# Optimization experiments

Measured on AMD Instinct MI355X. Metric: run time of the kernel, lower is better.

Reference implementation:

```python
import jax, jax.numpy as jnp
import numpy as np

IN_FEATURES = 4096
PADDED_DIM = 4096
K_HALF = PADDED_DIM // 2 + 1  # 2049
K = K_HALF
ALPHA_INIT = 1.0
INIT_SCALE = 0.1
BIAS_SCALE = 0.1
BATCH = 8192


def setup_inputs() -> dict:
    key = jax.random.key(0)
    kx, kr, ki, kb = jax.random.split(key, 4)
    x = jax.random.normal(kx, (BATCH, IN_FEATURES), dtype=jnp.float32)
    # Params initialized as in the module's __init__ (frequency-decayed scale)
    k_idx = jnp.arange(K_HALF, dtype=jnp.float32)
    prior_s = 1.0 / jnp.sqrt(1.0 + k_idx ** ALPHA_INIT)
    w_real = jax.random.normal(kr, (K_HALF,), dtype=jnp.float32) * (INIT_SCALE * prior_s)
    w_imag = jax.random.normal(ki, (K_HALF,), dtype=jnp.float32) * (INIT_SCALE * prior_s)
    w_imag = w_imag.at[0].set(0.0)
    w_imag = w_imag.at[-1].set(0.0)  # Nyquist bin (padded_dim even)
    bias = jax.random.normal(kb, (PADDED_DIM,), dtype=jnp.float32) * BIAS_SCALE
    return {"x": x, "w_real": w_real, "w_imag": w_imag, "bias": bias}


def _fourier_full(w_real, w_imag):
    # Mask frequencies >= K, then build full-length spectrum via Hermitian symmetry.
    mask = (jnp.arange(K_HALF) < K).astype(w_real.dtype)
    half = w_real * mask + 1j * (w_imag * mask)  # [k_half] complex
    nyq = half[-1].real[None].astype(half.dtype)  # real Nyquist bin
    full = jnp.concatenate([half[:-1], nyq, jnp.conj(half[1:-1])[::-1]])  # [padded_dim]
    return full


def reference(x, w_real, w_imag, bias):
    fft_full = _fourier_full(w_real, w_imag)  # [padded_dim] complex64
    # d_in == padded_dim -> no zero-padding needed (slice is a no-op, kept faithful)
    x_pad = x[..., :PADDED_DIM]
    Xf = jnp.fft.fft(x_pad, axis=-1)                 # [B, padded_dim] complex
    y = jnp.fft.ifft(Xf * fft_full[None, :], axis=-1).real  # [B, padded_dim]
    return y + bias[None, :]
```

## Files before the change

kernel.cpp:

```cpp
#include <hip/hip_runtime.h>
#include <math.h>

#define N 4096
#define THREADS 256
#define BATCH 8192

#define SWZ(i) ((i) ^ (((i) >> 4) & 15))
#define IDX16(p) ((((p) & 3) << 2) | ((p) >> 2))

__device__ __forceinline__ float2 cmul(float2 a, float2 b) {
    return make_float2(fmaf(a.x, b.x, -(a.y * b.y)), fmaf(a.x, b.y, a.y * b.x));
}

template<bool INV>
__device__ __forceinline__ void dft4(float2* v, int base, int stride) {
    float2 a = v[base], b = v[base + stride], c = v[base + 2 * stride], d = v[base + 3 * stride];
    float2 t0 = make_float2(a.x + c.x, a.y + c.y);
    float2 t1 = make_float2(a.x - c.x, a.y - c.y);
    float2 t2 = make_float2(b.x + d.x, b.y + d.y);
    float2 t3 = make_float2(b.x - d.x, b.y - d.y);
    float2 j3 = INV ? make_float2(-t3.y, t3.x) : make_float2(t3.y, -t3.x);
    v[base]              = make_float2(t0.x + t2.x, t0.y + t2.y);
    v[base + stride]     = make_float2(t1.x + j3.x, t1.y + j3.y);
    v[base + 2 * stride] = make_float2(t0.x - t2.x, t0.y - t2.y);
    v[base + 3 * stride] = make_float2(t1.x - j3.x, t1.y - j3.y);
}

template<bool INV>
__device__ __forceinline__ void tw16(float2* v) {
    const float C1 = 0.9238795325112867f;
    const float S1 = 0.3826834323650898f;
    const float R2 = 0.7071067811865476f;
    const float s = INV ? 1.0f : -1.0f;
    const float2 W1 = make_float2(C1, s * S1);
    const float2 W2 = make_float2(R2, s * R2);
    const float2 W3 = make_float2(S1, s * C1);
    const float2 W6 = make_float2(-R2, s * R2);
    const float2 W9 = make_float2(-C1, -s * S1);
    v[5]  = cmul(v[5],  W1);
    v[9]  = cmul(v[9],  W2);
    v[13] = cmul(v[13], W3);
    v[6]  = cmul(v[6],  W2);
    { float2 z = v[10]; v[10] = INV ? make_float2(-z.y, z.x) : make_float2(z.y, -z.x); }
    v[14] = cmul(v[14], W6);
    v[7]  = cmul(v[7],  W3);
    v[11] = cmul(v[11], W6);
    v[15] = cmul(v[15], W9);
}

template<bool INV>
__device__ __forceinline__ void dft16(float2* v) {
    #pragma unroll
    for (int n1 = 0; n1 < 4; ++n1) dft4<INV>(v, n1, 4);
    tw16<INV>(v);
    #pragma unroll
    for (int k2 = 0; k2 < 4; ++k2) dft4<INV>(v, 4 * k2, 1);
}

template<bool INV>
__device__ __forceinline__ void dft16_perm(float2* v) {
    #pragma unroll
    for (int n1 = 0; n1 < 4; ++n1) dft4<INV>(v, 4 * n1, 1);
    tw16<INV>(v);
    #pragma unroll
    for (int k2 = 0; k2 < 4; ++k2) dft4<INV>(v, k2, 4);
}

__global__ void prep_kernel(const float* __restrict__ wr, const float* __restrict__ wi,
                            float2* __restrict__ H, float2* __restrict__ tw) {
    int i = blockIdx.x * blockDim.x + threadIdx.x;
    if (i < N) {
        double ang = -2.0 * M_PI * (double)i / (double)N;
        tw[i] = make_float2((float)cos(ang), (float)sin(ang));
        float re, im;
        if (i <= N / 2) {
            re = wr[i];
            im = (i == N / 2) ? 0.0f : wi[i];
        } else {
            re = wr[N - i];
            im = -wi[N - i];
        }
        H[i] = make_float2(re, im);
    }
}

__global__ void prep_twA_kernel(float2* __restrict__ twA) {
    int i = blockIdx.x * blockDim.x + threadIdx.x;
    int p = i >> 8, t = i & 255;
    double ang = -2.0 * M_PI * (double)(t * p) / (double)N;
    twA[i] = make_float2((float)cos(ang), (float)sin(ang));
}

__global__ __launch_bounds__(THREADS, 2) void fft_conv_kernel(
        const float* __restrict__ x, const float2* __restrict__ H,
        const float2* __restrict__ tw, const float2* __restrict__ twA,
        const float* __restrict__ bias, float* __restrict__ out) {
    __shared__ float2 lds[2 * N];
    float2* __restrict__ ldsA = lds;
    float2* __restrict__ ldsB = lds + N;
    const int t = threadIdx.x;
    const long base1 = (long)(4 * blockIdx.x) * N;
    const long base2 = base1 + N;
    const long base3 = base1 + 2 * N;
    const long base4 = base1 + 3 * N;

    float2 va[16], vb[16];

    #pragma unroll
    for (int r = 0; r < 16; ++r) {
        va[r].x = x[base1 + t + 256 * r];
        va[r].y = x[base2 + t + 256 * r];
    }
    #pragma unroll
    for (int r = 0; r < 16; ++r) {
        vb[r].x = x[base3 + t + 256 * r];
        vb[r].y = x[base4 + t + 256 * r];
    }

    dft16<false>(va);
    dft16<false>(vb);
    #pragma unroll
    for (int p = 1; p < 16; ++p) {
        float2 w = twA[p * 256 + t];
        va[IDX16(p)] = cmul(va[IDX16(p)], w);
        vb[IDX16(p)] = cmul(vb[IDX16(p)], w);
    }
    #pragma unroll
    for (int p = 0; p < 16; ++p) ldsA[SWZ(16 * t + p)] = va[IDX16(p)];
    #pragma unroll
    for (int p = 0; p < 16; ++p) ldsB[SWZ(16 * t + p)] = vb[IDX16(p)];
    __syncthreads();

    #pragma unroll
    for (int r = 0; r < 16; ++r) va[r] = ldsA[SWZ(t + 256 * r)];
    #pragma unroll
    for (int r = 0; r < 16; ++r) vb[r] = ldsB[SWZ(t + 256 * r)];
    __syncthreads();
    dft16<false>(va);
    dft16<false>(vb);
    {
        const int k = t & 15, j = t >> 4;
        #pragma unroll
        for (int p = 1; p < 16; ++p) {
            float2 w = tw[16 * j * p];
            va[IDX16(p)] = cmul(va[IDX16(p)], w);
            vb[IDX16(p)] = cmul(vb[IDX16(p)], w);
        }
        #pragma unroll
        for (int p = 0; p < 16; ++p) ldsA[SWZ(k + 256 * j + 16 * p)] = va[IDX16(p)];
        #pragma unroll
        for (int p = 0; p < 16; ++p) ldsB[SWZ(k + 256 * j + 16 * p)] = vb[IDX16(p)];
    }
    __syncthreads();

    #pragma unroll
    for (int r = 0; r < 16; ++r) va[r] = ldsA[SWZ(t + 256 * r)];
    #pragma unroll
    for (int r = 0; r < 16; ++r) vb[r] = ldsB[SWZ(t + 256 * r)];
    __syncthreads();
    dft16<false>(va);
    dft16<false>(vb);
    #pragma unroll
    for (int q = 0; q < 16; ++q) {
        float2 h = H[t + 256 * IDX16(q)];
        va[q] = cmul(va[q], h);
        vb[q] = cmul(vb[q], h);
    }

    dft16_perm<true>(va);
    dft16_perm<true>(vb);
    #pragma unroll
    for (int p = 1; p < 16; ++p) {
        float2 w = twA[p * 256 + t]; w.y = -w.y;
        va[p] = cmul(va[p], w);
        vb[p] = cmul(vb[p], w);
    }
    #pragma unroll
    for (int p = 0; p < 16; ++p) ldsA[SWZ(16 * t + p)] = va[p];
    #pragma unroll
    for (int p = 0; p < 16; ++p) ldsB[SWZ(16 * t + p)] = vb[p];
    __syncthreads();

    #pragma unroll
    for (int r = 0; r < 16; ++r) va[r] = ldsA[SWZ(t + 256 * r)];
    #pragma unroll
    for (int r = 0; r < 16; ++r) vb[r] = ldsB[SWZ(t + 256 * r)];
    __syncthreads();
    dft16<true>(va);
    dft16<true>(vb);
    {
        const int k = t & 15, j = t >> 4;
        #pragma unroll
        for (int p = 1; p < 16; ++p) {
            float2 w = tw[16 * j * p]; w.y = -w.y;
            va[IDX16(p)] = cmul(va[IDX16(p)], w);
            vb[IDX16(p)] = cmul(vb[IDX16(p)], w);
        }
        #pragma unroll
        for (int p = 0; p < 16; ++p) ldsA[SWZ(k + 256 * j + 16 * p)] = va[IDX16(p)];
        #pragma unroll
        for (int p = 0; p < 16; ++p) ldsB[SWZ(k + 256 * j + 16 * p)] = vb[IDX16(p)];
    }
    __syncthreads();

    #pragma unroll
    for (int r = 0; r < 16; ++r) va[r] = ldsA[SWZ(t + 256 * r)];
    #pragma unroll
    for (int r = 0; r < 16; ++r) vb[r] = ldsB[SWZ(t + 256 * r)];
    dft16<true>(va);
    dft16<true>(vb);
    const float inv = 1.0f / (float)N;
    #pragma unroll
    for (int p = 0; p < 16; ++p) {
        float2 a = va[IDX16(p)];
        float2 b = vb[IDX16(p)];
        float bb = bias[t + 256 * p];
        out[base1 + t + 256 * p] = fmaf(a.x, inv, bb);
        out[base2 + t + 256 * p] = fmaf(a.y, inv, bb);
        out[base3 + t + 256 * p] = fmaf(b.x, inv, bb);
        out[base4 + t + 256 * p] = fmaf(b.y, inv, bb);
    }
}

extern "C" void kernel_launch(void* const* d_in, const int* in_sizes, int n_in,
                              void* d_out, int out_size, void* d_ws, size_t ws_size,
                              hipStream_t stream) {
    const float* x  = (const float*)d_in[0];
    const float* wr = (const float*)d_in[1];
    const float* wi = (const float*)d_in[2];
    const float* bs = (const float*)d_in[3];
    float* out = (float*)d_out;

    float2* H   = (float2*)d_ws;
    float2* tw  = (float2*)((char*)d_ws + (size_t)N * sizeof(float2));
    float2* twA = (float2*)((char*)d_ws + (size_t)2 * N * sizeof(float2));

    prep_kernel<<<dim3(N / THREADS), dim3(THREADS), 0, stream>>>(wr, wi, H, tw);
    prep_twA_kernel<<<dim3(N / THREADS), dim3(THREADS), 0, stream>>>(twA);
    fft_conv_kernel<<<dim3(BATCH / 4), dim3(THREADS), 0, stream>>>(x, H, tw, twA, bs, out);
}
```

Baseline: 263.7 us.

## Stagger the two FFT streams so LDS exchanges overlap the other stream's compute

Reorders the kernel so the A and B FFT pipelines run offset by half a stage. While one buffer passes through an LDS transpose and barrier, the other stream's radix-16 butterflies run. Each buffer now has its own barrier, which removes the extra post-read syncs. Correctness depends on the two LDS buffers being independent, and the longer live ranges could raise register pressure under the 2-blocks launch bound.

```diff
diff --git a/kernel.cpp b/kernel.cpp
--- a/kernel.cpp
+++ b/kernel.cpp
@@ -99,6 +99,7 @@
     float2* __restrict__ ldsA = lds;
     float2* __restrict__ ldsB = lds + N;
     const int t = threadIdx.x;
+    const int k = t & 15, j = t >> 4;
     const long base1 = (long)(4 * blockIdx.x) * N;
     const long base2 = base1 + N;
     const long base3 = base1 + 2 * N;
@@ -118,105 +119,116 @@
     }
 
     dft16<false>(va);
+    #pragma unroll
+    for (int p = 1; p < 16; ++p)
+        va[IDX16(p)] = cmul(va[IDX16(p)], twA[p * 256 + t]);
+    #pragma unroll
+    for (int p = 0; p < 16; ++p) ldsA[SWZ(16 * t + p)] = va[IDX16(p)];
+    __syncthreads();
+
+    #pragma unroll
+    for (int r = 0; r < 16; ++r) va[r] = ldsA[SWZ(t + 256 * r)];
     dft16<false>(vb);
     #pragma unroll
-    for (int p = 1; p < 16; ++p) {
-        float2 w = twA[p * 256 + t];
-        va[IDX16(p)] = cmul(va[IDX16(p)], w);
-        vb[IDX16(p)] = cmul(vb[IDX16(p)], w);
-    }
-    #pragma unroll
-    for (int p = 0; p < 16; ++p) ldsA[SWZ(16 * t + p)] = va[IDX16(p)];
+    for (int p = 1; p < 16; ++p)
+        vb[IDX16(p)] = cmul(vb[IDX16(p)], twA[p * 256 + t]);
     #pragma unroll
     for (int p = 0; p < 16; ++p) ldsB[SWZ(16 * t + p)] = vb[IDX16(p)];
     __syncthreads();
 
     #pragma unroll
-    for (int r = 0; r < 16; ++r) va[r] = ldsA[SWZ(t + 256 * r)];
-    #pragma unroll
-    for (int r = 0; r < 16; ++r) vb[r] = ldsB[SWZ(t + 256 * r)];
-    __syncthreads();
+    for (int r = 0; r < 16; ++r) vb[r] = ldsB[SWZ(t + 256 * r)];
     dft16<false>(va);
+    #pragma unroll
+    for (int p = 1; p < 16; ++p)
+        va[IDX16(p)] = cmul(va[IDX16(p)], tw[16 * j * p]);
+    #pragma unroll
+    for (int p = 0; p < 16; ++p) ldsA[SWZ(k + 256 * j + 16 * p)] = va[IDX16(p)];
+    __syncthreads();
+
+    #pragma unroll
+    for (int r = 0; r < 16; ++r) va[r] = ldsA[SWZ(t + 256 * r)];
     dft16<false>(vb);
-    {
-        const int k = t & 15, j = t >> 4;
-        #pragma unroll
-        for (int p = 1; p < 16; ++p) {
-            float2 w = tw[16 * j * p];
-            va[IDX16(p)] = cmul(va[IDX16(p)], w);
-            vb[IDX16(p)] = cmul(vb[IDX16(p)], w);
-        }
-        #pragma unroll
-        for (int p = 0; p < 16; ++p) ldsA[SWZ(k + 256 * j + 16 * p)] = va[IDX16(p)];
-        #pragma unroll
-        for (int p = 0; p < 16; ++p) ldsB[SWZ(k + 256 * j + 16 * p)] = vb[IDX16(p)];
-    }
-    __syncthreads();
-
-    #pragma unroll
-    for (int r = 0; r < 16; ++r) va[r] = ldsA[SWZ(t + 256 * r)];
-    #pragma unroll
-    for (int r = 0; r < 16; ++r) vb[r] = ldsB[SWZ(t + 256 * r)];
-    __syncthreads();
+    #pragma unroll
+    for (int p = 1; p < 16; ++p)
+        vb[IDX16(p)] = cmul(vb[IDX16(p)], tw[16 * j * p]);
+    #pragma unroll
+    for (int p = 0; p < 16; ++p) ldsB[SWZ(k + 256 * j + 16 * p)] = vb[IDX16(p)];
+    __syncthreads();
+
+    #pragma unroll
+    for (int r = 0; r < 16; ++r) vb[r] = ldsB[SWZ(t + 256 * r)];
     dft16<false>(va);
-    dft16<false>(vb);
-    #pragma unroll
-    for (int q = 0; q < 16; ++q) {
-        float2 h = H[t + 256 * IDX16(q)];
-        va[q] = cmul(va[q], h);
-        vb[q] = cmul(vb[q], h);
-    }
-
+    #pragma unroll
+    for (int q = 0; q < 16; ++q)
+        va[q] = cmul(va[q], H[t + 256 * IDX16(q)]);
     dft16_perm<true>(va);
-    dft16_perm<true>(vb);
     #pragma unroll
     for (int p = 1; p < 16; ++p) {
         float2 w = twA[p * 256 + t]; w.y = -w.y;
         va[p] = cmul(va[p], w);
+    }
+    #pragma unroll
+    for (int p = 0; p < 16; ++p) ldsA[SWZ(16 * t + p)] = va[p];
+    __syncthreads();
+
+    #pragma unroll
+    for (int r = 0; r < 16; ++r) va[r] = ldsA[SWZ(t + 256 * r)];
+    dft16<false>(vb);
+    #pragma unroll
+    for (int q = 0; q < 16; ++q)
+        vb[q] = cmul(vb[q], H[t + 256 * IDX16(q)]);
+    dft16_perm<true>(vb);
+    #pragma unroll
+    for (int p = 1; p < 16; ++p) {
+        float2 w = twA[p * 256 + t]; w.y = -w.y;
         vb[p] = cmul(vb[p], w);
     }
     #pragma unroll
-    for (int p = 0; p < 16; ++p) ldsA[SWZ(16 * t + p)] = va[p];
-    #pragma unroll
     for (int p = 0; p < 16; ++p) ldsB[SWZ(16 * t + p)] = vb[p];
     __syncthreads();
 
     #pragma unroll
-    for (int r = 0; r < 16; ++r) va[r] = ldsA[SWZ(t + 256 * r)];
-    #pragma unroll
-    for (int r = 0; r < 16; ++r) vb[r] = ldsB[SWZ(t + 256 * r)];
-    __syncthreads();
+    for (int r = 0; r < 16; ++r) vb[r] = ldsB[SWZ(t + 256 * r)];
     dft16<true>(va);
+    #pragma unroll
+    for (int p = 1; p < 16; ++p) {
+        float2 w = tw[16 * j * p]; w.y = -w.y;
+        va[IDX16(p)] = cmul(va[IDX16(p)], w);
+    }
+    #pragma unroll
+    for (int p = 0; p < 16; ++p) ldsA[SWZ(k + 256 * j + 16 * p)] = va[IDX16(p)];
+    __syncthreads();
+
+    #pragma unroll
+    for (int r = 0; r < 16; ++r) va[r] = ldsA[SWZ(t + 256 * r)];
     dft16<true>(vb);
-    {
-        const int k = t & 15, j = t >> 4;
-        #pragma unroll
-        for (int p = 1; p < 16; ++p) {
-            float2 w = tw[16 * j * p]; w.y = -w.y;
-            va[IDX16(p)] = cmul(va[IDX16(p)], w);
-            vb[IDX16(p)] = cmul(vb[IDX16(p)], w);
-        }
-        #pragma unroll
-        for (int p = 0; p < 16; ++p) ldsA[SWZ(k + 256 * j + 16 * p)] = va[IDX16(p)];
-        #pragma unroll
-        for (int p = 0; p < 16; ++p) ldsB[SWZ(k + 256 * j + 16 * p)] = vb[IDX16(p)];
-    }
-    __syncthreads();
-
-    #pragma unroll
-    for (int r = 0; r < 16; ++r) va[r] = ldsA[SWZ(t + 256 * r)];
+    #pragma unroll
+    for (int p = 1; p < 16; ++p) {
+        float2 w = tw[16 * j * p]; w.y = -w.y;
+        vb[IDX16(p)] = cmul(vb[IDX16(p)], w);
+    }
+    #pragma unroll
+    for (int p = 0; p < 16; ++p) ldsB[SWZ(k + 256 * j + 16 * p)] = vb[IDX16(p)];
+    __syncthreads();
+
     #pragma unroll
     for (int r = 0; r < 16; ++r) vb[r] = ldsB[SWZ(t + 256 * r)];
     dft16<true>(va);
-    dft16<true>(vb);
     const float inv = 1.0f / (float)N;
     #pragma unroll
     for (int p = 0; p < 16; ++p) {
         float2 a = va[IDX16(p)];
-        float2 b = vb[IDX16(p)];
         float bb = bias[t + 256 * p];
         out[base1 + t + 256 * p] = fmaf(a.x, inv, bb);
         out[base2 + t + 256 * p] = fmaf(a.y, inv, bb);
+    }
+
+    dft16<true>(vb);
+    #pragma unroll
+    for (int p = 0; p < 16; ++p) {
+        float2 b = vb[IDX16(p)];
+        float bb = bias[t + 256 * p];
         out[base3 + t + 256 * p] = fmaf(b.x, inv, bb);
         out[base4 + t + 256 * p] = fmaf(b.y, inv, bb);
     }
```

Result: slower. 274.2 us (+4.0%).

## Make FFT-conv kernel persistent and prefetch next batch rows into registers

Applied to the files above, without the earlier changes.

The grid shrinks to 512 blocks, and each block loops over 4 groups of four rows. While the first LDS transpose of the current group is in flight, the block issues global loads for the next group into a separate register set (pa/pb). The goal is to hide global-memory latency behind compute. The cost is 64 extra float2 registers per thread, which may push register use past the occupancy target of 2 blocks per CU and cause spills. It also removes the wave-level parallelism that came from having more blocks.

```diff
diff --git a/kernel.cpp b/kernel.cpp
--- a/kernel.cpp
+++ b/kernel.cpp
@@ -4,6 +4,8 @@
 #define N 4096
 #define THREADS 256
 #define BATCH 8192
+#define GRID 512
+#define ITERS ((BATCH / 4) / GRID)
 
 #define SWZ(i) ((i) ^ (((i) >> 4) & 15))
 #define IDX16(p) ((((p) & 3) << 2) | ((p) >> 2))
@@ -99,47 +101,67 @@
     float2* __restrict__ ldsA = lds;
     float2* __restrict__ ldsB = lds + N;
     const int t = threadIdx.x;
-    const long base1 = (long)(4 * blockIdx.x) * N;
-    const long base2 = base1 + N;
-    const long base3 = base1 + 2 * N;
-    const long base4 = base1 + 3 * N;
-
+    const int k = t & 15, j = t >> 4;
+
+    float2 pa[16], pb[16];
     float2 va[16], vb[16];
 
-    #pragma unroll
-    for (int r = 0; r < 16; ++r) {
-        va[r].x = x[base1 + t + 256 * r];
-        va[r].y = x[base2 + t + 256 * r];
+    long g = blockIdx.x;
+
+    {
+        const long b1 = (long)(4 * g) * N, b2 = b1 + N, b3 = b1 + 2 * N, b4 = b1 + 3 * N;
+        #pragma unroll
+        for (int r = 0; r < 16; ++r) {
+            pa[r].x = x[b1 + t + 256 * r];
+            pa[r].y = x[b2 + t + 256 * r];
+        }
+        #pragma unroll
+        for (int r = 0; r < 16; ++r) {
+            pb[r].x = x[b3 + t + 256 * r];
+            pb[r].y = x[b4 + t + 256 * r];
+        }
     }
-    #pragma unroll
-    for (int r = 0; r < 16; ++r) {
-        vb[r].x = x[base3 + t + 256 * r];
-        vb[r].y = x[base4 + t + 256 * r];
-    }
-
-    dft16<false>(va);
-    dft16<false>(vb);
-    #pragma unroll
-    for (int p = 1; p < 16; ++p) {
-        float2 w = twA[p * 256 + t];
-        va[IDX16(p)] = cmul(va[IDX16(p)], w);
-        vb[IDX16(p)] = cmul(vb[IDX16(p)], w);
-    }
-    #pragma unroll
-    for (int p = 0; p < 16; ++p) ldsA[SWZ(16 * t + p)] = va[IDX16(p)];
-    #pragma unroll
-    for (int p = 0; p < 16; ++p) ldsB[SWZ(16 * t + p)] = vb[IDX16(p)];
-    __syncthreads();
-
-    #pragma unroll
-    for (int r = 0; r < 16; ++r) va[r] = ldsA[SWZ(t + 256 * r)];
-    #pragma unroll
-    for (int r = 0; r < 16; ++r) vb[r] = ldsB[SWZ(t + 256 * r)];
-    __syncthreads();
-    dft16<false>(va);
-    dft16<false>(vb);
-    {
-        const int k = t & 15, j = t >> 4;
+
+    #pragma unroll 1
+    for (int it = 0; it < ITERS; ++it) {
+        const long b1 = (long)(4 * g) * N, b2 = b1 + N, b3 = b1 + 2 * N, b4 = b1 + 3 * N;
+
+        dft16<false>(pa);
+        dft16<false>(pb);
+        #pragma unroll
+        for (int p = 1; p < 16; ++p) {
+            float2 w = twA[p * 256 + t];
+            pa[IDX16(p)] = cmul(pa[IDX16(p)], w);
+            pb[IDX16(p)] = cmul(pb[IDX16(p)], w);
+        }
+        #pragma unroll
+        for (int p = 0; p < 16; ++p) ldsA[SWZ(16 * t + p)] = pa[IDX16(p)];
+        #pragma unroll
+        for (int p = 0; p < 16; ++p) ldsB[SWZ(16 * t + p)] = pb[IDX16(p)];
+
+        if (it + 1 < ITERS) {
+            const long ng = g + GRID;
+            const long n1 = (long)(4 * ng) * N, n2 = n1 + N, n3 = n1 + 2 * N, n4 = n1 + 3 * N;
+            #pragma unroll
+            for (int r = 0; r < 16; ++r) {
+                pa[r].x = x[n1 + t + 256 * r];
+                pa[r].y = x[n2 + t + 256 * r];
+            }
+            #pragma unroll
+            for (int r = 0; r < 16; ++r) {
+                pb[r].x = x[n3 + t + 256 * r];
+                pb[r].y = x[n4 + t + 256 * r];
+            }
+        }
+        __syncthreads();
+
+        #pragma unroll
+        for (int r = 0; r < 16; ++r) va[r] = ldsA[SWZ(t + 256 * r)];
+        #pragma unroll
+        for (int r = 0; r < 16; ++r) vb[r] = ldsB[SWZ(t + 256 * r)];
+        __syncthreads();
+        dft16<false>(va);
+        dft16<false>(vb);
         #pragma unroll
         for (int p = 1; p < 16; ++p) {
             float2 w = tw[16 * j * p];
@@ -150,46 +172,42 @@
         for (int p = 0; p < 16; ++p) ldsA[SWZ(k + 256 * j + 16 * p)] = va[IDX16(p)];
         #pragma unroll
         for (int p = 0; p < 16; ++p) ldsB[SWZ(k + 256 * j + 16 * p)] = vb[IDX16(p)];
-    }
-    __syncthreads();
-
-    #pragma unroll
-    for (int r = 0; r < 16; ++r) va[r] = ldsA[SWZ(t + 256 * r)];
-    #pragma unroll
-    for (int r = 0; r < 16; ++r) vb[r] = ldsB[SWZ(t + 256 * r)];
-    __syncthreads();
-    dft16<false>(va);
-    dft16<false>(vb);
-    #pragma unroll
-    for (int q = 0; q < 16; ++q) {
-        float2 h = H[t + 256 * IDX16(q)];
-        va[q] = cmul(va[q], h);
-        vb[q] = cmul(vb[q], h);
-    }
-
-    dft16_perm<true>(va);
-    dft16_perm<true>(vb);
-    #pragma unroll
-    for (int p = 1; p < 16; ++p) {
-        float2 w = twA[p * 256 + t]; w.y = -w.y;
-        va[p] = cmul(va[p], w);
-        vb[p] = cmul(vb[p], w);
-    }
-    #pragma unroll
-    for (int p = 0; p < 16; ++p) ldsA[SWZ(16 * t + p)] = va[p];
-    #pragma unroll
-    for (int p = 0; p < 16; ++p) ldsB[SWZ(16 * t + p)] = vb[p];
-    __syncthreads();
-
-    #pragma unroll
-    for (int r = 0; r < 16; ++r) va[r] = ldsA[SWZ(t + 256 * r)];
-    #pragma unroll
-    for (int r = 0; r < 16; ++r) vb[r] = ldsB[SWZ(t + 256 * r)];
-    __syncthreads();
-    dft16<true>(va);
-    dft16<true>(vb);
-    {
-        const int k = t & 15, j = t >> 4;
+        __syncthreads();
+
+        #pragma unroll
+        for (int r = 0; r < 16; ++r) va[r] = ldsA[SWZ(t + 256 * r)];
+        #pragma unroll
+        for (int r = 0; r < 16; ++r) vb[r] = ldsB[SWZ(t + 256 * r)];
+        __syncthreads();
+        dft16<false>(va);
+        dft16<false>(vb);
+        #pragma unroll
+        for (int q = 0; q < 16; ++q) {
+            float2 h = H[t + 256 * IDX16(q)];
+            va[q] = cmul(va[q], h);
+            vb[q] = cmul(vb[q], h);
+        }
+        dft16_perm<true>(va);
+        dft16_perm<true>(vb);
+        #pragma unroll
+        for (int p = 1; p < 16; ++p) {
+            float2 w = twA[p * 256 + t]; w.y = -w.y;
+            va[p] = cmul(va[p], w);
+            vb[p] = cmul(vb[p], w);
+        }
+        #pragma unroll
+        for (int p = 0; p < 16; ++p) ldsA[SWZ(16 * t + p)] = va[p];
+        #pragma unroll
+        for (int p = 0; p < 16; ++p) ldsB[SWZ(16 * t + p)] = vb[p];
+        __syncthreads();
+
+        #pragma unroll
+        for (int r = 0; r < 16; ++r) va[r] = ldsA[SWZ(t + 256 * r)];
+        #pragma unroll
+        for (int r = 0; r < 16; ++r) vb[r] = ldsB[SWZ(t + 256 * r)];
+        __syncthreads();
+        dft16<true>(va);
+        dft16<true>(vb);
         #pragma unroll
         for (int p = 1; p < 16; ++p) {
             float2 w = tw[16 * j * p]; w.y = -w.y;
@@ -200,25 +218,27 @@
         for (int p = 0; p < 16; ++p) ldsA[SWZ(k + 256 * j + 16 * p)] = va[IDX16(p)];
         #pragma unroll
         for (int p = 0; p < 16; ++p) ldsB[SWZ(k + 256 * j + 16 * p)] = vb[IDX16(p)];
-    }
-    __syncthreads();
-
-    #pragma unroll
-    for (int r = 0; r < 16; ++r) va[r] = ldsA[SWZ(t + 256 * r)];
-    #pragma unroll
-    for (int r = 0; r < 16; ++r) vb[r] = ldsB[SWZ(t + 256 * r)];
-    dft16<true>(va);
-    dft16<true>(vb);
-    const float inv = 1.0f / (float)N;
-    #pragma unroll
-    for (int p = 0; p < 16; ++p) {
-        float2 a = va[IDX16(p)];
-        float2 b = vb[IDX16(p)];
-        float bb = bias[t + 256 * p];
-        out[base1 + t + 256 * p] = fmaf(a.x, inv, bb);
-        out[base2 + t + 256 * p] = fmaf(a.y, inv, bb);
-        out[base3 + t + 256 * p] = fmaf(b.x, inv, bb);
-        out[base4 + t + 256 * p] = fmaf(b.y, inv, bb);
+        __syncthreads();
+
+        #pragma unroll
+        for (int r = 0; r < 16; ++r) va[r] = ldsA[SWZ(t + 256 * r)];
+        #pragma unroll
+        for (int r = 0; r < 16; ++r) vb[r] = ldsB[SWZ(t + 256 * r)];
+        dft16<true>(va);
+        dft16<true>(vb);
+        const float inv = 1.0f / (float)N;
+        #pragma unroll
+        for (int p = 0; p < 16; ++p) {
+            float2 a = va[IDX16(p)];
+            float2 b = vb[IDX16(p)];
+            float bb = bias[t + 256 * p];
+            out[b1 + t + 256 * p] = fmaf(a.x, inv, bb);
+            out[b2 + t + 256 * p] = fmaf(a.y, inv, bb);
+            out[b3 + t + 256 * p] = fmaf(b.x, inv, bb);
+            out[b4 + t + 256 * p] = fmaf(b.y, inv, bb);
+        }
+        __syncthreads();
+        g += GRID;
     }
 }
 
@@ -237,5 +257,5 @@
 
     prep_kernel<<<dim3(N / THREADS), dim3(THREADS), 0, stream>>>(wr, wi, H, tw);
     prep_twA_kernel<<<dim3(N / THREADS), dim3(THREADS), 0, stream>>>(twA);
-    fft_conv_kernel<<<dim3(BATCH / 4), dim3(THREADS), 0, stream>>>(x, H, tw, twA, bs, out);
-}
+    fft_conv_kernel<<<dim3(GRID), dim3(THREADS), 0, stream>>>(x, H, tw, twA, bs, out);
+}
```

After: 484.4 us. +83.7%, slower.
